# Kernel tuning notes

Hardware: AMD Instinct MI355X
Metric: run time of the kernel (lower is better)

## Reference

```python
import jax, jax.numpy as jnp
import numpy as np

D_MODEL = 1024
NUM_HEADS = 16
NUM_KV_HEADS = 4
HEAD_DIM = D_MODEL // NUM_HEADS  # 64
KV_DIM = HEAD_DIM * NUM_KV_HEADS  # 256
B, N = 2, 2048


def setup_inputs() -> dict:
    key = jax.random.key(0)
    ks = jax.random.split(key, 7)
    std = 1.0 / np.sqrt(D_MODEL)
    return {
        "x": jax.random.normal(ks[0], (B, N, D_MODEL), dtype=jnp.float32),
        "cos": jax.random.uniform(ks[1], (N, HEAD_DIM // 2), dtype=jnp.float32),
        "sin": jax.random.uniform(ks[2], (N, HEAD_DIM // 2), dtype=jnp.float32),
        "Wq": jax.random.normal(ks[3], (D_MODEL, D_MODEL), dtype=jnp.float32) * std,
        "Wk": jax.random.normal(ks[4], (D_MODEL, KV_DIM), dtype=jnp.float32) * std,
        "Wv": jax.random.normal(ks[5], (D_MODEL, KV_DIM), dtype=jnp.float32) * std,
        "Wo": jax.random.normal(ks[6], (D_MODEL, D_MODEL), dtype=jnp.float32) * std,
    }


def _rope(t, cos, sin):
    # t: [B, H, N, head_dim]; cos/sin: [N, head_dim//2]
    t1, t2 = t[..., ::2], t[..., 1::2]
    c = cos[None, None]
    s = sin[None, None]
    # NOTE: halves are concatenated (not re-interleaved), faithful to source.
    return jnp.concatenate([t1 * c - t2 * s, t1 * s + t2 * c], axis=-1)


def reference(x, cos, sin, Wq, Wk, Wv, Wo):
    b, n, d = x.shape
    scale = HEAD_DIM ** -0.5
    q = (x @ Wq).reshape(b, n, NUM_HEADS, HEAD_DIM).transpose(0, 2, 1, 3)
    k = (x @ Wk).reshape(b, n, NUM_KV_HEADS, HEAD_DIM).transpose(0, 2, 1, 3)
    v = (x @ Wv).reshape(b, n, NUM_KV_HEADS, HEAD_DIM).transpose(0, 2, 1, 3)
    q = _rope(q, cos, sin)
    k = _rope(k, cos, sin)
    num_rep = NUM_HEADS // NUM_KV_HEADS
    k = jnp.repeat(k, num_rep, axis=1)  # [b, H, n, hd]
    v = jnp.repeat(v, num_rep, axis=1)
    attn = jnp.einsum("bhqd,bhkd->bhqk", q, k) * scale
    attn = jax.nn.softmax(attn, axis=-1)
    out = jnp.einsum("bhqk,bhkd->bhqd", attn, v)
    out = out.transpose(0, 2, 1, 3).reshape(b, n, d)
    return out @ Wo
```

## Files before the change

### kernel.cpp

```cpp
#include <hip/hip_runtime.h>
#include <math.h>

#define D_MODEL 1024
#define NHEADS  16
#define NKV     4
#define HDIM    64
#define KVDIM   256
#define BB      2
#define NN      2048
#define MROWS   (BB*NN)
#define QKVN    1536
#define NTASK   (MROWS*NHEADS)
#define NSPLIT  2
#define KVBLK   128
#define NTILE   ((NN/NSPLIT)/KVBLK)

typedef unsigned short ushort_t;
typedef unsigned int uint_t;
typedef float    f32x4 __attribute__((ext_vector_type(4)));
typedef _Float16 h16x8 __attribute__((ext_vector_type(8)));
typedef _Float16 h16x4 __attribute__((ext_vector_type(4)));
typedef __fp16   fp16x2 __attribute__((ext_vector_type(2)));

#define MFMAH(A,B,C)  __builtin_amdgcn_mfma_f32_16x16x32_f16((A),(B),(C),0,0,0)
#define MFMA16(A,B,C) __builtin_amdgcn_mfma_f32_16x16x16f16((A),(B),(C),0,0,0)
#define EXP2(x) __builtin_amdgcn_exp2f(x)

#define GLDS(gp, lp) __builtin_amdgcn_global_load_lds( \
    (const __attribute__((address_space(1))) void*)(gp), \
    (__attribute__((address_space(3))) void*)(lp), 16, 0, 0)

__device__ __forceinline__ ushort_t f2h(float f) {
    _Float16 h = (_Float16)f;
    return *(ushort_t*)&h;
}
__device__ __forceinline__ float h2f(ushort_t u) {
    return (float)(*(const _Float16*)&u);
}
__device__ __forceinline__ uint_t pk2h(float a, float b) {
    fp16x2 v = __builtin_amdgcn_cvt_pkrtz(a, b);
    return *(uint_t*)&v;
}

__global__ __launch_bounds__(256)
void prep_kernel(const float* __restrict__ x, const float* __restrict__ Wq,
                 const float* __restrict__ Wk, const float* __restrict__ Wv,
                 const float* __restrict__ Wo, ushort_t* __restrict__ xb,
                 ushort_t* __restrict__ WqkvT, ushort_t* __restrict__ WoT)
{
    __shared__ float T[32][33];
    int blk = blockIdx.x;
    if (blk < 4096) {
        const int i = blk * 256 + threadIdx.x;
        float4 v = ((const float4*)x)[i];
        uint2 o;
        o.x = pk2h(v.x, v.y);
        o.y = pk2h(v.z, v.w);
        ((uint2*)xb)[i] = o;
        return;
    }
    blk -= 4096;
    const float* src; ushort_t* dst; int N, bx, by;
    if (blk < 1024)      { src = Wq; dst = WqkvT;                            N = D_MODEL; bx = blk & 31; by = blk >> 5; }
    else if (blk < 1280) { blk -= 1024; src = Wk; dst = WqkvT + (size_t)1024 * D_MODEL; N = KVDIM; bx = blk & 7; by = blk >> 3; }
    else if (blk < 1536) { blk -= 1280; src = Wv; dst = WqkvT + (size_t)1280 * D_MODEL; N = KVDIM; bx = blk & 7; by = blk >> 3; }
    else                 { blk -= 1536; src = Wo; dst = WoT;                 N = D_MODEL; bx = blk & 31; by = blk >> 5; }
    const int tx = threadIdx.x & 31, ty = threadIdx.x >> 5;
    const int n0 = bx * 32, k0 = by * 32;
#pragma unroll
    for (int i = 0; i < 4; i++)
        T[ty + i * 8][tx] = src[(size_t)(k0 + ty + i * 8) * N + n0 + tx];
    __syncthreads();
#pragma unroll
    for (int i = 0; i < 4; i++)
        dst[(size_t)(n0 + ty + i * 8) * D_MODEL + k0 + tx] = f2h(T[tx][ty + i * 8]);
}

#define NKW (MROWS*NKV*32)
#define NKBLK (NKW / 256)
__global__ __launch_bounds__(256)
void ropevt_kernel(const ushort_t* __restrict__ QKVh, const float* __restrict__ Cos,
                   const float* __restrict__ Sin, ushort_t* __restrict__ Kb,
                   ushort_t* __restrict__ Vt)
{
    __shared__ ushort_t T[32][34];
    if (blockIdx.x >= NKBLK) {
        const int blk2 = blockIdx.x - NKBLK;
        const int bx = blk2 & 63, by = (blk2 >> 6) & 7, b = blk2 >> 9;
        const int tx = threadIdx.x & 31, ty = threadIdx.x >> 5;
        const int n0 = bx * 32, d0 = by * 32;
#pragma unroll
        for (int i = 0; i < 4; i++)
            T[ty + i * 8][tx] =
                QKVh[(size_t)(b * NN + n0 + ty + i * 8) * QKVN + 1280 + d0 + tx];
        __syncthreads();
#pragma unroll
        for (int i = 0; i < 4; i++)
            Vt[(size_t)(b * 256 + d0 + ty + i * 8) * NN + n0 + tx] = T[tx][ty + i * 8];
        return;
    }
    const int i2 = blockIdx.x * 256 + threadIdx.x;
    const int row = i2 >> 7, rem = i2 & 127;
    const int h = rem >> 5, j = rem & 31;
    const int b = row >> 11, n = row & (NN - 1);
    const uint_t pr = *(const uint_t*)&QKVh[(size_t)row * QKVN + 1024 + h * 64 + 2 * j];
    const float e = h2f((ushort_t)pr), o = h2f((ushort_t)(pr >> 16));
    const float c = Cos[n * 32 + j], s = Sin[n * 32 + j];
    ushort_t* dst = Kb + ((size_t)(b * 4 + h) * NN + n) * 64;
    dst[j]      = f2h(e * c - o * s);
    dst[j + 32] = f2h(e * s + o * c);
}

__global__ __launch_bounds__(256)
void gemm_qkv(const ushort_t* __restrict__ A, const ushort_t* __restrict__ Bt,
              ushort_t* __restrict__ C, int M, int N, int K)
{
    __shared__ ushort_t As[4][128 * 32];
    __shared__ ushort_t Bs[4][64 * 32];

    const int tid  = threadIdx.x;
    const int wave = tid >> 6, lane = tid & 63;
    const int quad = lane >> 4, l16 = lane & 15;
    const int rowBase = blockIdx.y * 128, colBase = blockIdx.x * 64;
    const int wm = (wave >> 1) * 64, wn = (wave & 1) * 32;

    f32x4 acc[4][2];
    const f32x4 zz = {0.f, 0.f, 0.f, 0.f};
#pragma unroll
    for (int i = 0; i < 4; i++)
#pragma unroll
        for (int j = 0; j < 2; j++) acc[i][j] = zz;

    const int sr = wave * 32 + (lane >> 2);
    const int sc = ((lane & 3) ^ ((lane >> 3) & 3)) * 8;
    const ushort_t* Ag0 = A + (size_t)(rowBase + sr) * K + sc;
    const ushort_t* Ag1 = A + (size_t)(rowBase + sr + 16) * K + sc;
    const int segA0 = (wave * 2 + 0) * 512, segA1 = (wave * 2 + 1) * 512;
    const int br = wave * 16 + (lane >> 2);
    const ushort_t* Bg0 = Bt + (size_t)(colBase + br) * K + sc;
    const int segB = wave * 512;

    const int fcol = (quad ^ ((l16 >> 1) & 3)) * 8;

    GLDS(Ag0, &As[0][segA0]);
    GLDS(Ag1, &As[0][segA1]);
    GLDS(Bg0, &Bs[0][segB]);
    GLDS(Ag0 + 32, &As[1][segA0]);
    GLDS(Ag1 + 32, &As[1][segA1]);
    GLDS(Bg0 + 32, &Bs[1][segB]);

#define QKV_COMPUTE(curslot, koff) { \
        h16x8 af[4], bf[2]; \
        _Pragma("unroll") \
        for (int mt = 0; mt < 4; mt++) \
            af[mt] = *(const h16x8*)&As[curslot][(wm + mt * 16 + l16) * 32 + fcol]; \
        _Pragma("unroll") \
        for (int nt = 0; nt < 2; nt++) \
            bf[nt] = *(const h16x8*)&Bs[curslot][(wn + nt * 16 + l16) * 32 + fcol]; \
        _Pragma("unroll") \
        for (int mt = 0; mt < 4; mt++) \
            _Pragma("unroll") \
            for (int nt = 0; nt < 2; nt++) \
                acc[mt][nt] = MFMAH(af[mt], bf[nt], acc[mt][nt]); \
    }

    for (int k0 = 0; k0 < K; k0 += 64) {
        const int s0 = (k0 >> 5) & 3, s1 = (s0 + 1) & 3;
        const int s2 = (s0 + 2) & 3, s3 = (s0 + 3) & 3;
        __syncthreads();
        if (k0 + 64 < K) {
            GLDS(Ag0 + k0 + 64, &As[s2][segA0]);
            GLDS(Ag1 + k0 + 64, &As[s2][segA1]);
            GLDS(Bg0 + k0 + 64, &Bs[s2][segB]);
        }
        if (k0 + 96 < K) {
            GLDS(Ag0 + k0 + 96, &As[s3][segA0]);
            GLDS(Ag1 + k0 + 96, &As[s3][segA1]);
            GLDS(Bg0 + k0 + 96, &Bs[s3][segB]);
        }
        QKV_COMPUTE(s0, k0);
        QKV_COMPUTE(s1, k0 + 32);
    }
#undef QKV_COMPUTE

#pragma unroll
    for (int mt = 0; mt < 4; mt++)
#pragma unroll
        for (int nt = 0; nt < 2; nt++) {
            const int row = rowBase + wm + mt * 16 + quad * 4;
            const int col = colBase + wn + nt * 16 + l16;
#pragma unroll
            for (int r = 0; r < 4; r++)
                C[(size_t)(row + r) * N + col] = f2h(acc[mt][nt][r]);
        }
}

__global__ __launch_bounds__(256)
void attn_mfma(const ushort_t* __restrict__ QKVh, const float* __restrict__ Cos,
               const float* __restrict__ Sin, const ushort_t* __restrict__ Kb,
               const ushort_t* __restrict__ Vt, ushort_t* __restrict__ Pnum,
               float* __restrict__ Pl)
{
    const int qt = blockIdx.x, h = blockIdx.y;
    const int b = blockIdx.z >> 1, chunk = blockIdx.z & 1;
    const int kvh = h >> 2;
    const int tid = threadIdx.x;
    const int wave = tid >> 6, lane = tid & 63;
    const int quad = lane >> 4, l16 = lane & 15;

    __shared__ ushort_t Ks[128][72];
    __shared__ ushort_t Vs[64][136];

    const int row0 = qt * 256 + wave * 64;
    const float SC = 0.125f * 1.44269504f;

    h16x8 qf[4][2];
#pragma unroll
    for (int mt = 0; mt < 4; mt++) {
        const int n = row0 + mt * 16 + l16;
        const uint_t* pr =
            (const uint_t*)(QKVh + (size_t)(b * NN + n) * QKVN + h * 64) + quad * 8;
        uint4 pa = *(const uint4*)pr;
        uint4 pc = *(const uint4*)(pr + 4);
        const uint_t pk[8] = {pa.x, pa.y, pa.z, pa.w, pc.x, pc.y, pc.z, pc.w};
        const float4 c0 = *(const float4*)&Cos[(size_t)n * 32 + quad * 8];
        const float4 c1 = *(const float4*)&Cos[(size_t)n * 32 + quad * 8 + 4];
        const float4 s0 = *(const float4*)&Sin[(size_t)n * 32 + quad * 8];
        const float4 s1 = *(const float4*)&Sin[(size_t)n * 32 + quad * 8 + 4];
        const float cc[8] = {c0.x, c0.y, c0.z, c0.w, c1.x, c1.y, c1.z, c1.w};
        const float ss[8] = {s0.x, s0.y, s0.z, s0.w, s1.x, s1.y, s1.z, s1.w};
#pragma unroll
        for (int i = 0; i < 8; i++) {
            const float e = h2f((ushort_t)pk[i]);
            const float o = h2f((ushort_t)(pk[i] >> 16));
            qf[mt][0][i] = (_Float16)((e * cc[i] - o * ss[i]) * SC);
            qf[mt][1][i] = (_Float16)((e * ss[i] + o * cc[i]) * SC);
        }
    }

    h16x4 ones;
#pragma unroll
    for (int i = 0; i < 4; i++) ones[i] = (_Float16)1.0f;

    const ushort_t* kbase = Kb + (size_t)(b * 4 + kvh) * NN * 64;
    const ushort_t* vbase = Vt + (size_t)(b * 256 + kvh * 64) * NN;
    const int key_lo = chunk * (NN / NSPLIT);
    const int rot = (qt + ((h & 3) << 2)) & (NTILE - 1);

    const int srow = tid >> 2, sseg = (tid & 3) * 8;
    const ushort_t* kp_lane = kbase + (size_t)srow * 64 + sseg;
    const ushort_t* vp_lane = vbase + (size_t)srow * NN + sseg;

    const f32x4 zz = {0.f, 0.f, 0.f, 0.f};
    f32x4 o[4][4];
#pragma unroll
    for (int mt = 0; mt < 4; mt++)
#pragma unroll
        for (int dt = 0; dt < 4; dt++) o[mt][dt] = zz;
    f32x4 lsum[4];
#pragma unroll
    for (int mt = 0; mt < 4; mt++) lsum[mt] = zz;

    const int key0 = key_lo + rot * KVBLK;
    uint4 kreg0 = *(const uint4*)(kp_lane + (size_t)key0 * 64);
    uint4 kreg1 = *(const uint4*)(kp_lane + (size_t)key0 * 64 + 32);
    uint4 kreg2 = *(const uint4*)(kp_lane + (size_t)(key0 + 64) * 64);
    uint4 kreg3 = *(const uint4*)(kp_lane + (size_t)(key0 + 64) * 64 + 32);
    uint4 vreg0 = *(const uint4*)(vp_lane + key0);
    uint4 vreg1 = *(const uint4*)(vp_lane + key0 + 32);
    uint4 vreg2 = *(const uint4*)(vp_lane + key0 + 64);
    uint4 vreg3 = *(const uint4*)(vp_lane + key0 + 96);

    for (int t = 0; t < NTILE; t++) {
        __syncthreads();
        *(uint4*)&Ks[srow][sseg]           = kreg0;
        *(uint4*)&Ks[srow][sseg + 32]      = kreg1;
        *(uint4*)&Ks[srow + 64][sseg]      = kreg2;
        *(uint4*)&Ks[srow + 64][sseg + 32] = kreg3;
        *(uint4*)&Vs[srow][sseg]           = vreg0;
        *(uint4*)&Vs[srow][sseg + 32]      = vreg1;
        *(uint4*)&Vs[srow][sseg + 64]      = vreg2;
        *(uint4*)&Vs[srow][sseg + 96]      = vreg3;
        __syncthreads();

        if (t < NTILE - 1) {
            const int kn = key_lo + ((rot + t + 1) & (NTILE - 1)) * KVBLK;
            kreg0 = *(const uint4*)(kp_lane + (size_t)kn * 64);
            kreg1 = *(const uint4*)(kp_lane + (size_t)kn * 64 + 32);
            kreg2 = *(const uint4*)(kp_lane + (size_t)(kn + 64) * 64);
            kreg3 = *(const uint4*)(kp_lane + (size_t)(kn + 64) * 64 + 32);
            vreg0 = *(const uint4*)(vp_lane + kn);
            vreg1 = *(const uint4*)(vp_lane + kn + 32);
            vreg2 = *(const uint4*)(vp_lane + kn + 64);
            vreg3 = *(const uint4*)(vp_lane + kn + 96);
        }

#pragma unroll
        for (int kt = 0; kt < 8; kt++) {
            h16x8 kf0 = *(const h16x8*)&Ks[kt * 16 + l16][quad * 8];
            h16x8 kf1 = *(const h16x8*)&Ks[kt * 16 + l16][32 + quad * 8];
            h16x4 va[4];
#pragma unroll
            for (int dt = 0; dt < 4; dt++)
                va[dt] = *(const h16x4*)&Vs[dt * 16 + l16][kt * 16 + quad * 4];

            uint2 pb[4];
#pragma unroll
            for (int mt = 0; mt < 4; mt++) {
                f32x4 st = MFMAH(kf0, qf[mt][0], zz);
                st = MFMAH(kf1, qf[mt][1], st);
                pb[mt].x = pk2h(EXP2(st[0]), EXP2(st[1]));
                pb[mt].y = pk2h(EXP2(st[2]), EXP2(st[3]));
            }
#pragma unroll
            for (int mt = 0; mt < 4; mt++) {
                const h16x4 pbv = *(const h16x4*)&pb[mt];
#pragma unroll
                for (int dt = 0; dt < 4; dt++)
                    o[mt][dt] = MFMA16(va[dt], pbv, o[mt][dt]);
                lsum[mt] = MFMA16(ones, pbv, lsum[mt]);
            }
        }
    }

    const size_t task0 = (size_t)(b * 16 + h) * NN + row0;
    ushort_t* np = Pnum + ((size_t)chunk * NTASK + task0) * 64;
#pragma unroll
    for (int mt = 0; mt < 4; mt++) {
        const float lt = lsum[mt][0];
        const float inv = 1.0f / lt;
#pragma unroll
        for (int dt = 0; dt < 4; dt++) {
            f32x4 v = o[mt][dt];
            uint2 pk;
            pk.x = pk2h(v[0] * inv, v[1] * inv);
            pk.y = pk2h(v[2] * inv, v[3] * inv);
            *(uint2*)&np[(size_t)(mt * 16 + l16) * 64 + dt * 16 + quad * 4] = pk;
        }
        if (quad == 0)
            Pl[(size_t)chunk * NTASK + task0 + mt * 16 + l16] = lt;
    }
}

__global__ __launch_bounds__(256)
void combine_kernel(const ushort_t* __restrict__ Pnum, const float* __restrict__ Pl,
                    ushort_t* __restrict__ Ob)
{
    const uint_t i = blockIdx.x * 256 + threadIdx.x;
    const int row = i >> 7;
    const int g = i & 127;
    const int col0 = g * 8;
    const int h = col0 >> 6, d = col0 & 63;
    const int b = row >> 11, n = row & (NN - 1);
    const size_t task = ((size_t)(b * 16 + h) << 11) + n;

    float l[NSPLIT], tot = 0.f;
#pragma unroll
    for (int c = 0; c < NSPLIT; c++) { l[c] = Pl[(size_t)c * NTASK + task]; tot += l[c]; }
    const float inv = 1.f / tot;

    uint4 in[NSPLIT];
#pragma unroll
    for (int c = 0; c < NSPLIT; c++)
        in[c] = *(const uint4*)&Pnum[((size_t)c * NTASK + task) * 64 + d];

    uint4 out;
    uint_t* po = (uint_t*)&out;
#pragma unroll
    for (int j = 0; j < 4; j++) {
        float x = 0.f, y = 0.f;
#pragma unroll
        for (int c = 0; c < NSPLIT; c++) {
            const float w = l[c] * inv;
            fp16x2 u = *(const fp16x2*)&((const uint_t*)&in[c])[j];
            x += w * (float)u.x;
            y += w * (float)u.y;
        }
        po[j] = pk2h(x, y);
    }
    *(uint4*)&Ob[(size_t)row * D_MODEL + col0] = out;
}

__global__ __launch_bounds__(256)
void gemm_wo(const ushort_t* __restrict__ A, const ushort_t* __restrict__ Bt,
             float* __restrict__ C)
{
    __shared__ ushort_t As[4][128 * 32];
    __shared__ ushort_t Bs[4][64 * 32];

    const int tid  = threadIdx.x;
    const int wave = tid >> 6, lane = tid & 63;
    const int quad = lane >> 4, l16 = lane & 15;
    const int rowBase = blockIdx.y * 128, colBase = blockIdx.x * 64;
    const int wm = (wave >> 1) * 64, wn = (wave & 1) * 32;

    f32x4 acc[4][2];
    const f32x4 zz = {0.f, 0.f, 0.f, 0.f};
#pragma unroll
    for (int i = 0; i < 4; i++)
#pragma unroll
        for (int j = 0; j < 2; j++) acc[i][j] = zz;

    const int sr = wave * 32 + (lane >> 2);
    const int sc = ((lane & 3) ^ ((lane >> 3) & 3)) * 8;
    const ushort_t* Ag0 = A + (size_t)(rowBase + sr) * D_MODEL + sc;
    const ushort_t* Ag1 = A + (size_t)(rowBase + sr + 16) * D_MODEL + sc;
    const int segA0 = (wave * 2 + 0) * 512, segA1 = (wave * 2 + 1) * 512;
    const int br = wave * 16 + (lane >> 2);
    const ushort_t* Bg0 = Bt + (size_t)(colBase + br) * D_MODEL + sc;
    const int segB = wave * 512;

    const int fcol = (quad ^ ((l16 >> 1) & 3)) * 8;

    GLDS(Ag0, &As[0][segA0]);
    GLDS(Ag1, &As[0][segA1]);
    GLDS(Bg0, &Bs[0][segB]);
    GLDS(Ag0 + 32, &As[1][segA0]);
    GLDS(Ag1 + 32, &As[1][segA1]);
    GLDS(Bg0 + 32, &Bs[1][segB]);

#define WO_COMPUTE(curslot) { \
        h16x8 af[4], bf[2]; \
        _Pragma("unroll") \
        for (int mt = 0; mt < 4; mt++) \
            af[mt] = *(const h16x8*)&As[curslot][(wm + mt * 16 + l16) * 32 + fcol]; \
        _Pragma("unroll") \
        for (int nt = 0; nt < 2; nt++) \
            bf[nt] = *(const h16x8*)&Bs[curslot][(wn + nt * 16 + l16) * 32 + fcol]; \
        _Pragma("unroll") \
        for (int mt = 0; mt < 4; mt++) \
            _Pragma("unroll") \
            for (int nt = 0; nt < 2; nt++) \
                acc[mt][nt] = MFMAH(af[mt], bf[nt], acc[mt][nt]); \
    }

    for (int k0 = 0; k0 < D_MODEL; k0 += 64) {
        const int s0 = (k0 >> 5) & 3, s1 = (s0 + 1) & 3;
        const int s2 = (s0 + 2) & 3, s3 = (s0 + 3) & 3;
        __syncthreads();
        if (k0 + 64 < D_MODEL) {
            GLDS(Ag0 + k0 + 64, &As[s2][segA0]);
            GLDS(Ag1 + k0 + 64, &As[s2][segA1]);
            GLDS(Bg0 + k0 + 64, &Bs[s2][segB]);
        }
        if (k0 + 96 < D_MODEL) {
            GLDS(Ag0 + k0 + 96, &As[s3][segA0]);
            GLDS(Ag1 + k0 + 96, &As[s3][segA1]);
            GLDS(Bg0 + k0 + 96, &Bs[s3][segB]);
        }
        WO_COMPUTE(s0);
        WO_COMPUTE(s1);
    }
#undef WO_COMPUTE

#pragma unroll
    for (int mt = 0; mt < 4; mt++)
#pragma unroll
        for (int nt = 0; nt < 2; nt++) {
            const int row = rowBase + wm + mt * 16 + quad * 4;
            const int col = colBase + wn + nt * 16 + l16;
#pragma unroll
            for (int r = 0; r < 4; r++)
                C[(size_t)(row + r) * D_MODEL + col] = acc[mt][nt][r];
        }
}

extern "C" void kernel_launch(void* const* d_in, const int* in_sizes, int n_in,
                              void* d_out, int out_size, void* d_ws, size_t ws_size,
                              hipStream_t stream)
{
    const float* x    = (const float*)d_in[0];
    const float* cosp = (const float*)d_in[1];
    const float* sinp = (const float*)d_in[2];
    const float* Wq   = (const float*)d_in[3];
    const float* Wk   = (const float*)d_in[4];
    const float* Wv   = (const float*)d_in[5];
    const float* Wo   = (const float*)d_in[6];

    char* w = (char*)d_ws;
    ushort_t* xb     = (ushort_t*)w;                       w += (size_t)MROWS * D_MODEL * 2;
    ushort_t* WqkvT  = (ushort_t*)w;                       w += (size_t)QKVN * D_MODEL * 2;
    ushort_t* WoT    = (ushort_t*)w;                       w += (size_t)D_MODEL * D_MODEL * 2;
    ushort_t* QKVh   = (ushort_t*)w;                       w += (size_t)MROWS * QKVN * 2;
    ushort_t* Kbuf   = (ushort_t*)w;                       w += (size_t)MROWS * KVDIM * 2;
    ushort_t* Vt     = (ushort_t*)w;                       w += (size_t)MROWS * KVDIM * 2;
    ushort_t* Obuf   = (ushort_t*)w;                       w += (size_t)MROWS * D_MODEL * 2;
    ushort_t* Pnum   = (ushort_t*)w;                       w += (size_t)NSPLIT * NTASK * 64 * 2;
    float*    Pl     = (float*)w;

    prep_kernel<<<6656, 256, 0, stream>>>(x, Wq, Wk, Wv, Wo, xb, WqkvT, WoT);

    gemm_qkv<<<dim3(QKVN / 64, MROWS / 128), 256, 0, stream>>>(
        xb, WqkvT, QKVh, MROWS, QKVN, D_MODEL);

    ropevt_kernel<<<NKBLK + 1024, 256, 0, stream>>>(
        QKVh, cosp, sinp, Kbuf, Vt);

    attn_mfma<<<dim3(NN / 256, NHEADS, BB * NSPLIT), 256, 0, stream>>>(
        QKVh, cosp, sinp, Kbuf, Vt, Pnum, Pl);

    combine_kernel<<<(MROWS * D_MODEL / 8) / 256, 256, 0, stream>>>(
        Pnum, Pl, Obuf);

    gemm_wo<<<dim3(D_MODEL / 64, MROWS / 128), 256, 0, stream>>>(
        Obuf, WoT, (float*)d_out);
}
```

Before: 185.0 us.

## Double-buffer attention K/V tiles via direct global-to-LDS loads with XOR swizzle

```diff
diff --git a/kernel.cpp b/kernel.cpp
--- a/kernel.cpp
+++ b/kernel.cpp
@@ -149,7 +149,7 @@
     GLDS(Ag1 + 32, &As[1][segA1]);
     GLDS(Bg0 + 32, &Bs[1][segB]);
 
-#define QKV_COMPUTE(curslot, koff) { \
+#define QKV_COMPUTE(curslot) { \
         h16x8 af[4], bf[2]; \
         _Pragma("unroll") \
         for (int mt = 0; mt < 4; mt++) \
@@ -178,8 +178,8 @@
             GLDS(Ag1 + k0 + 96, &As[s3][segA1]);
             GLDS(Bg0 + k0 + 96, &Bs[s3][segB]);
         }
-        QKV_COMPUTE(s0, k0);
-        QKV_COMPUTE(s1, k0 + 32);
+        QKV_COMPUTE(s0);
+        QKV_COMPUTE(s1);
     }
 #undef QKV_COMPUTE
 
@@ -208,8 +208,8 @@
     const int wave = tid >> 6, lane = tid & 63;
     const int quad = lane >> 4, l16 = lane & 15;
 
-    __shared__ ushort_t Ks[128][72];
-    __shared__ ushort_t Vs[64][136];
+    __shared__ ushort_t Ks[2][128][64];
+    __shared__ ushort_t Vs[2][64][128];
 
     const int row0 = qt * 256 + wave * 64;
     const float SC = 0.125f * 1.44269504f;
@@ -247,9 +247,20 @@
     const int key_lo = chunk * (NN / NSPLIT);
     const int rot = (qt + ((h & 3) << 2)) & (NTILE - 1);
 
-    const int srow = tid >> 2, sseg = (tid & 3) * 8;
-    const ushort_t* kp_lane = kbase + (size_t)srow * 64 + sseg;
-    const ushort_t* vp_lane = vbase + (size_t)srow * NN + sseg;
+    const int krow = (wave << 3) + (lane >> 3);
+    const int kseg = (lane & 7) ^ (krow & 7);
+    const ushort_t* kp_lane = kbase + (size_t)krow * 64 + kseg * 8;
+    const int vrow = (wave << 2) + (lane >> 4);
+    const int vseg = (lane & 15) ^ (vrow & 7);
+    const ushort_t* vp_lane = vbase + (size_t)vrow * NN + vseg * 8;
+
+#define STAGE(key, bufidx) { \
+        _Pragma("unroll") \
+        for (int i = 0; i < 4; i++) { \
+            GLDS(kp_lane + (size_t)((key) + i * 32) * 64, &Ks[bufidx][i * 32 + (wave << 3)][0]); \
+            GLDS(vp_lane + (size_t)(i * 16) * NN + (key), &Vs[bufidx][i * 16 + (wave << 2)][0]); \
+        } \
+    }
 
     const f32x4 zz = {0.f, 0.f, 0.f, 0.f};
     f32x4 o[4][4];
@@ -261,48 +272,27 @@
 #pragma unroll
     for (int mt = 0; mt < 4; mt++) lsum[mt] = zz;
 
-    const int key0 = key_lo + rot * KVBLK;
-    uint4 kreg0 = *(const uint4*)(kp_lane + (size_t)key0 * 64);
-    uint4 kreg1 = *(const uint4*)(kp_lane + (size_t)key0 * 64 + 32);
-    uint4 kreg2 = *(const uint4*)(kp_lane + (size_t)(key0 + 64) * 64);
-    uint4 kreg3 = *(const uint4*)(kp_lane + (size_t)(key0 + 64) * 64 + 32);
-    uint4 vreg0 = *(const uint4*)(vp_lane + key0);
-    uint4 vreg1 = *(const uint4*)(vp_lane + key0 + 32);
-    uint4 vreg2 = *(const uint4*)(vp_lane + key0 + 64);
-    uint4 vreg3 = *(const uint4*)(vp_lane + key0 + 96);
+    STAGE(key_lo + rot * KVBLK, 0);
+
+    const int kswz = l16 & 7;
 
     for (int t = 0; t < NTILE; t++) {
+        const int cur = t & 1, nxt = cur ^ 1;
         __syncthreads();
-        *(uint4*)&Ks[srow][sseg]           = kreg0;
-        *(uint4*)&Ks[srow][sseg + 32]      = kreg1;
-        *(uint4*)&Ks[srow + 64][sseg]      = kreg2;
-        *(uint4*)&Ks[srow + 64][sseg + 32] = kreg3;
-        *(uint4*)&Vs[srow][sseg]           = vreg0;
-        *(uint4*)&Vs[srow][sseg + 32]      = vreg1;
-        *(uint4*)&Vs[srow][sseg + 64]      = vreg2;
-        *(uint4*)&Vs[srow][sseg + 96]      = vreg3;
-        __syncthreads();
-
         if (t < NTILE - 1) {
             const int kn = key_lo + ((rot + t + 1) & (NTILE - 1)) * KVBLK;
-            kreg0 = *(const uint4*)(kp_lane + (size_t)kn * 64);
-            kreg1 = *(const uint4*)(kp_lane + (size_t)kn * 64 + 32);
-            kreg2 = *(const uint4*)(kp_lane + (size_t)(kn + 64) * 64);
-            kreg3 = *(const uint4*)(kp_lane + (size_t)(kn + 64) * 64 + 32);
-            vreg0 = *(const uint4*)(vp_lane + kn);
-            vreg1 = *(const uint4*)(vp_lane + kn + 32);
-            vreg2 = *(const uint4*)(vp_lane + kn + 64);
-            vreg3 = *(const uint4*)(vp_lane + kn + 96);
+            STAGE(kn, nxt);
         }
 
 #pragma unroll
         for (int kt = 0; kt < 8; kt++) {
-            h16x8 kf0 = *(const h16x8*)&Ks[kt * 16 + l16][quad * 8];
-            h16x8 kf1 = *(const h16x8*)&Ks[kt * 16 + l16][32 + quad * 8];
+            h16x8 kf0 = *(const h16x8*)&Ks[cur][kt * 16 + l16][(quad ^ kswz) << 3];
+            h16x8 kf1 = *(const h16x8*)&Ks[cur][kt * 16 + l16][((4 + quad) ^ kswz) << 3];
             h16x4 va[4];
 #pragma unroll
             for (int dt = 0; dt < 4; dt++)
-                va[dt] = *(const h16x4*)&Vs[dt * 16 + l16][kt * 16 + quad * 4];
+                va[dt] = *(const h16x4*)&Vs[cur][dt * 16 + l16]
+                    [(((kt * 2 + (quad >> 1)) ^ kswz) << 3) + ((quad & 1) << 2)];
 
             uint2 pb[4];
 #pragma unroll
@@ -322,6 +312,7 @@
             }
         }
     }
+#undef STAGE
 
     const size_t task0 = (size_t)(b * 16 + h) * NN + row0;
     ushort_t* np = Pnum + ((size_t)chunk * NTASK + task0) * 64;
```

Result: no change. 185.8 us (+0.5%).
